# Optimization experiments

Hardware: AMD Instinct MI355X
Metric: run time of the kernel (lower is better)

The kernel has to match this reference:

```python
import jax, jax.numpy as jnp
import numpy as np

B, D_IMG, D_TXT, E = 4096, 768, 768, 512
LAMBDA_CMP = 1.0
EPS = 1e-10


def setup_inputs() -> dict:
    key = jax.random.key(0)
    k1, k2, k3, k4, k5 = jax.random.split(key, 5)
    return {
        "images": jax.random.normal(k1, (B, D_IMG), dtype=jnp.float32),
        "texts": jax.random.normal(k2, (B, D_TXT), dtype=jnp.float32),
        "labels": jax.random.randint(k3, (B,), 0, 1000, dtype=jnp.int32),
        "W_img": jax.random.normal(k4, (D_IMG, E), dtype=jnp.float32) / np.sqrt(D_IMG),
        "W_txt": jax.random.normal(k5, (D_TXT, E), dtype=jnp.float32) / np.sqrt(D_TXT),
        "logit_scale": jnp.asarray(np.log(1.0 / 0.07), dtype=jnp.float32),
    }


def reference(images, texts, labels, W_img, W_txt, logit_scale):
    # CLIP-style encoders: linear project + L2 normalize
    img = images @ W_img
    txt = texts @ W_txt
    img = img / jnp.linalg.norm(img, axis=-1, keepdims=True)
    txt = txt / jnp.linalg.norm(txt, axis=-1, keepdims=True)
    logits = jnp.exp(logit_scale) * (img @ txt.T)  # [B, B]

    b = logits.shape[0]
    rows = jnp.arange(b)
    logp = jax.nn.log_softmax(logits, axis=-1)
    clip_loss = -jnp.mean(logp[rows, labels])

    probs = jnp.exp(logp)                # softmax probs [B, B]
    p_yi = probs[rows, labels]           # [B]
    # columns j whose label differs from sample i's label AND prob exceeds p_yi
    diff_label = labels[None, :] != labels[:, None]           # [B, B]
    mask = diff_label & (probs > p_yi[:, None])               # [B, B]
    denom = jnp.sum(jnp.where(mask, probs, 0.0), axis=1)      # [B]
    has_any = jnp.any(mask, axis=1)
    cmp_loss = jnp.sum(jnp.where(has_any, p_yi / (denom + EPS), 0.0)) / b

    return clip_loss + LAMBDA_CMP * cmp_loss
```

## Files before the change

kernel.cpp:

```cpp
#include <hip/hip_runtime.h>
#include <stdint.h>

#define BATCH 4096
#define DDIM  768
#define EDIM  512
#define NSPLIT 16
#define LOG2E 1.44269504088896340736f

using short8  = __attribute__((ext_vector_type(8))) short;
using float4v = __attribute__((ext_vector_type(4))) float;

__device__ __forceinline__ unsigned short f2bf(float x) {
    union { float f; uint32_t u; } v; v.f = x;
    uint32_t u = v.u;
    u += 0x7FFFu + ((u >> 16) & 1u);
    return (unsigned short)(u >> 16);
}
__device__ __forceinline__ float bf2f(unsigned short h) {
    union { uint32_t u; float f; } v; v.u = ((uint32_t)h) << 16;
    return v.f;
}

__device__ __forceinline__ void gl2lds16(const void* g, void* l) {
    __builtin_amdgcn_global_load_lds(
        (const __attribute__((address_space(1))) void*)g,
        (__attribute__((address_space(3))) void*)l, 16, 0, 0);
}

__global__ void cvt2(const float* __restrict__ a, const float* __restrict__ b,
                     unsigned short* __restrict__ oa, unsigned short* __restrict__ ob) {
    int i = blockIdx.x * 256 + threadIdx.x;
    const float* in = blockIdx.y ? b : a;
    unsigned short* out = blockIdx.y ? ob : oa;
    float4 v = ((const float4*)in)[i];
    ushort4 o;
    o.x = f2bf(v.x); o.y = f2bf(v.y); o.z = f2bf(v.z); o.w = f2bf(v.w);
    ((ushort4*)out)[i] = o;
}

__global__ void transpose2(const float* __restrict__ Wa, const float* __restrict__ Wb,
                           unsigned short* __restrict__ Ta, unsigned short* __restrict__ Tb) {
    const float* W = blockIdx.z ? Wb : Wa;
    unsigned short* Wt = blockIdx.z ? Tb : Ta;
    __shared__ float tile[32][33];
    int n0 = blockIdx.x * 32, k0 = blockIdx.y * 32;
    int tid = threadIdx.x;
    for (int p = 0; p < 4; ++p) {
        int e = tid + p * 256; int lr = e >> 5, lc = e & 31;
        tile[lc][lr] = W[(size_t)(k0 + lr) * EDIM + n0 + lc];
    }
    __syncthreads();
    for (int p = 0; p < 4; ++p) {
        int e = tid + p * 256; int lr = e >> 5, lc = e & 31;
        Wt[(size_t)(n0 + lr) * DDIM + k0 + lc] = f2bf(tile[lr][lc]);
    }
}

__global__ __launch_bounds__(256) void gemm_nt(const unsigned short* __restrict__ Aimg,
                                               const unsigned short* __restrict__ Atxt,
                                               const unsigned short* __restrict__ Bimg,
                                               const unsigned short* __restrict__ Btxt,
                                               unsigned short* __restrict__ Cimg,
                                               unsigned short* __restrict__ Ctxt) {
    const unsigned short* A  = blockIdx.z ? Atxt : Aimg;
    const unsigned short* Bm = blockIdx.z ? Btxt : Bimg;
    unsigned short* C        = blockIdx.z ? Ctxt : Cimg;
    __shared__ __align__(16) unsigned short As[2 * 128 * 32];
    __shared__ __align__(16) unsigned short Bs[2 * 64 * 32];
    int tid = threadIdx.x;
    int wave = tid >> 6, lane = tid & 63;
    int q = lane >> 4, r = lane & 15;
    int m0 = blockIdx.x * 128, n0 = blockIdx.y * 64;
    int sw = (r >> 1) & 3;

    const unsigned short* gsA[4];
    unsigned short* lsA[4];
    for (int i = 0; i < 4; ++i) {
        int u = i * 256 + tid;
        int kc2 = u >> 9, row = (u >> 2) & 127, kq = u & 3;
        int kq2 = kq ^ ((row >> 1) & 3);
        gsA[i] = &A[(size_t)(m0 + row) * DDIM + kc2 * 32 + kq2 * 8];
        lsA[i] = &As[u * 8];
    }
    const unsigned short* gsB[2];
    unsigned short* lsB[2];
    for (int i = 0; i < 2; ++i) {
        int u = i * 256 + tid;
        int kc2 = u >> 8, row = (u >> 2) & 63, kq = u & 3;
        int kq2 = kq ^ ((row >> 1) & 3);
        gsB[i] = &Bm[(size_t)(n0 + row) * DDIM + kc2 * 32 + kq2 * 8];
        lsB[i] = &Bs[u * 8];
    }

    float4v acc[2][4];
    for (int a = 0; a < 2; ++a)
        for (int t = 0; t < 4; ++t) acc[a][t] = (float4v){0.f, 0.f, 0.f, 0.f};

    for (int it = 0; it < DDIM / 64; ++it) {
        int k0 = it * 64;
        __syncthreads();
        for (int i = 0; i < 4; ++i) gl2lds16(gsA[i] + k0, lsA[i]);
        for (int i = 0; i < 2; ++i) gl2lds16(gsB[i] + k0, lsB[i]);
        __syncthreads();
        for (int kc2 = 0; kc2 < 2; ++kc2) {
            short8 a0 = *(const short8*)&As[kc2 * 4096 + (wave * 32 + r) * 32 + (q ^ sw) * 8];
            short8 a1 = *(const short8*)&As[kc2 * 4096 + (wave * 32 + 16 + r) * 32 + (q ^ sw) * 8];
            for (int t = 0; t < 4; ++t) {
                short8 b = *(const short8*)&Bs[kc2 * 2048 + (t * 16 + r) * 32 + (q ^ sw) * 8];
                acc[0][t] = __builtin_amdgcn_mfma_f32_16x16x32_bf16(a0, b, acc[0][t], 0, 0, 0);
                acc[1][t] = __builtin_amdgcn_mfma_f32_16x16x32_bf16(a1, b, acc[1][t], 0, 0, 0);
            }
        }
    }
    for (int rg = 0; rg < 2; ++rg)
        for (int t = 0; t < 4; ++t)
            for (int g = 0; g < 4; ++g)
                C[(size_t)(m0 + wave * 32 + rg * 16 + q * 4 + g) * EDIM + n0 + t * 16 + r] =
                    f2bf(acc[rg][t][g]);
}

__global__ void norm_rows(unsigned short* __restrict__ Pa, unsigned short* __restrict__ Pb) {
    unsigned short* P = blockIdx.y ? Pb : Pa;
    int wave = threadIdx.x >> 6, lane = threadIdx.x & 63;
    int row = blockIdx.x * 4 + wave;
    unsigned short* p = &P[(size_t)row * 512 + lane * 8];
    union { unsigned short us[8]; uint4 u4; } v;
    v.u4 = *(const uint4*)p;
    float f[8], s = 0.f;
    for (int j = 0; j < 8; ++j) { f[j] = bf2f(v.us[j]); s += f[j] * f[j]; }
    for (int off = 1; off < 64; off <<= 1) s += __shfl_xor(s, off);
    float rn = rsqrtf(s);
    for (int j = 0; j < 8; ++j) v.us[j] = f2bf(f[j] * rn);
    *(uint4*)p = v.u4;
}

__global__ void tdot(const unsigned short* __restrict__ img, const unsigned short* __restrict__ txt,
                     const int* __restrict__ labels, float* __restrict__ tout) {
    int wave = threadIdx.x >> 6, lane = threadIdx.x & 63;
    int row = blockIdx.x * 4 + wave;
    int lab = labels[row];
    union { unsigned short us[8]; uint4 u4; } a, b;
    a.u4 = *(const uint4*)&img[(size_t)row * 512 + lane * 8];
    b.u4 = *(const uint4*)&txt[(size_t)lab * 512 + lane * 8];
    float s = 0.f;
    for (int j = 0; j < 8; ++j) s += bf2f(a.us[j]) * bf2f(b.us[j]);
    for (int off = 1; off < 64; off <<= 1) s += __shfl_xor(s, off);
    if (lane == 0) tout[row] = s;
}

__global__ __launch_bounds__(256) void flash_pass(
    const unsigned short* __restrict__ img, const unsigned short* __restrict__ txt,
    const int* __restrict__ labels, const float* __restrict__ tvals,
    const float* __restrict__ ls,
    float* __restrict__ lP, float* __restrict__ dP) {
    __shared__ __align__(16) unsigned short Bs[8 * 64 * 32];
    int tid = threadIdx.x;
    int wave = tid >> 6, lane = tid & 63;
    int q = lane >> 4, r = lane & 15;
    int row0 = blockIdx.x * 128 + wave * 32;
    int split = blockIdx.y;
    float alpha = expf(ls[0]);
    float c1 = alpha * LOG2E;

    int srow = tid >> 2, skp = tid & 3;
    int skp2 = skp ^ ((srow >> 1) & 3);
    int sw = (r >> 1) & 3;

    short8 af[2][16];
    for (int rg = 0; rg < 2; ++rg)
        for (int kc = 0; kc < 16; ++kc)
            af[rg][kc] = *(const short8*)&img[(size_t)(row0 + rg * 16 + r) * 512 + kc * 32 + q * 8];

    int labr[8]; float tr[8];
    for (int rg = 0; rg < 2; ++rg)
        for (int g = 0; g < 4; ++g) {
            int rw = row0 + rg * 16 + q * 4 + g;
            labr[rg * 4 + g] = labels[rw];
            tr[rg * 4 + g] = tvals[rw];
        }
    float l[8] = {0.f}, d[8] = {0.f};

    for (int ct = 0; ct < 4; ++ct) {
        int colbase = split * 256 + ct * 64;
        const unsigned short* gB = &txt[(size_t)(colbase + srow) * 512 + skp2 * 8];
        float4v acc[2][4];
        for (int rg = 0; rg < 2; ++rg)
            for (int t = 0; t < 4; ++t) acc[rg][t] = (float4v){0.f, 0.f, 0.f, 0.f};
        for (int h = 0; h < 2; ++h) {
            __syncthreads();
            for (int i = 0; i < 8; ++i)
                gl2lds16(gB + h * 256 + i * 32, &Bs[i * 2048 + tid * 8]);
            __syncthreads();
            for (int kc = 0; kc < 8; ++kc) {
                short8 a0 = af[0][h * 8 + kc];
                short8 a1 = af[1][h * 8 + kc];
                for (int t = 0; t < 4; ++t) {
                    short8 bf = *(const short8*)&Bs[(kc * 64 + t * 16 + r) * 32 + (q ^ sw) * 8];
                    acc[0][t] = __builtin_amdgcn_mfma_f32_16x16x32_bf16(a0, bf, acc[0][t], 0, 0, 0);
                    acc[1][t] = __builtin_amdgcn_mfma_f32_16x16x32_bf16(a1, bf, acc[1][t], 0, 0, 0);
                }
            }
        }
        for (int t = 0; t < 4; ++t) {
            int lc = labels[colbase + t * 16 + r];
            for (int rg = 0; rg < 2; ++rg)
                for (int g = 0; g < 4; ++g) {
                    float a = acc[rg][t][g];
                    float p = exp2f(fmaf(a, c1, -c1));
                    int ix = rg * 4 + g;
                    l[ix] += p;
                    d[ix] += ((a > tr[ix]) && (lc != labr[ix])) ? p : 0.f;
                }
        }
    }
    for (int ix = 0; ix < 8; ++ix) {
        float lv = l[ix], dv = d[ix];
        for (int off = 1; off < 16; off <<= 1) {
            lv += __shfl_xor(lv, off);
            dv += __shfl_xor(dv, off);
        }
        if (r == 0) {
            int rw = row0 + (ix >> 2) * 16 + q * 4 + (ix & 3);
            lP[(size_t)rw * NSPLIT + split] = lv;
            dP[(size_t)rw * NSPLIT + split] = dv;
        }
    }
}

__global__ void combine(const float* __restrict__ lP, const float* __restrict__ dP,
                        const float* __restrict__ tvals, const float* __restrict__ ls,
                        float* __restrict__ out) {
    int row = blockIdx.x * 256 + threadIdx.x;
    float alpha = expf(ls[0]);
    float L = 0.f, D = 0.f;
    for (int s = 0; s < NSPLIT; ++s) {
        L += lP[(size_t)row * NSPLIT + s];
        D += dP[(size_t)row * NSPLIT + s];
    }
    float tm = alpha * (tvals[row] - 1.0f);
    float clip = logf(L) - tm;
    float py = expf(tm) / L;
    float cmp = (D > 0.f) ? py / (D / L + 1e-10f) : 0.f;
    float v = clip + cmp;
    for (int off = 1; off < 64; off <<= 1) v += __shfl_xor(v, off);
    __shared__ float w4[4];
    int wave = threadIdx.x >> 6, lane = threadIdx.x & 63;
    if (lane == 0) w4[wave] = v;
    __syncthreads();
    if (threadIdx.x == 0)
        atomicAdd(out, (w4[0] + w4[1] + w4[2] + w4[3]) * (1.0f / BATCH));
}

extern "C" void kernel_launch(void* const* d_in, const int* in_sizes, int n_in,
                              void* d_out, int out_size, void* d_ws, size_t ws_size,
                              hipStream_t stream) {
    const float* images = (const float*)d_in[0];
    const float* texts  = (const float*)d_in[1];
    const int*   labels = (const int*)d_in[2];
    const float* W_img  = (const float*)d_in[3];
    const float* W_txt  = (const float*)d_in[4];
    const float* lscale = (const float*)d_in[5];
    float* out = (float*)d_out;

    char* ws = (char*)d_ws;
    unsigned short* img_bf = (unsigned short*)(ws + 0);
    unsigned short* txt_bf = (unsigned short*)(ws + 6291456);
    unsigned short* wt_img = (unsigned short*)(ws + 12582912);
    unsigned short* wt_txt = (unsigned short*)(ws + 13369344);
    unsigned short* proj_i = (unsigned short*)(ws + 14155776);
    unsigned short* proj_t = (unsigned short*)(ws + 18350080);
    float*          lP     = (float*)(ws + 0);
    float*          dP     = (float*)(ws + 262144);
    float*          tvals  = (float*)(ws + 524288);

    hipMemsetAsync(out, 0, sizeof(float), stream);
    cvt2<<<dim3(3072, 2), 256, 0, stream>>>(images, texts, img_bf, txt_bf);
    transpose2<<<dim3(EDIM / 32, DDIM / 32, 2), 256, 0, stream>>>(W_img, W_txt, wt_img, wt_txt);
    gemm_nt<<<dim3(BATCH / 128, EDIM / 64, 2), 256, 0, stream>>>(img_bf, txt_bf, wt_img, wt_txt,
                                                                 proj_i, proj_t);
    norm_rows<<<dim3(BATCH / 4, 2), 256, 0, stream>>>(proj_i, proj_t);
    tdot<<<BATCH / 4, 256, 0, stream>>>(proj_i, proj_t, labels, tvals);
    flash_pass<<<dim3(BATCH / 128, NSPLIT), 256, 0, stream>>>(proj_i, proj_t, labels, tvals, lscale,
                                                              lP, dP);
    combine<<<16, 256, 0, stream>>>(lP, dP, tvals, lscale, out);
}
```

Before: 143.6 us.

## Merge prep kernels, double flash splits, and store partials split-major

Fuses the bf16 conversion and the weight transpose into one prep kernel to save a launch. It doubles the column splits in the flash pass (32 splits of 128 columns each), which doubles the grid to 1024 blocks to improve occupancy and latency hiding. The partial sums are now stored split-major so the combine kernel reads them coalesced. In exchange, each block reloads the A fragments for half as much work, and the combine step reads twice as many partials.

Measured after the change: 170.0 us. 1.18x slower.

```diff
diff --git a/kernel.cpp b/kernel.cpp
--- a/kernel.cpp
+++ b/kernel.cpp
@@ -4,7 +4,7 @@
 #define BATCH 4096
 #define DDIM  768
 #define EDIM  512
-#define NSPLIT 16
+#define NSPLIT 32
 #define LOG2E 1.44269504088896340736f
 
 using short8  = __attribute__((ext_vector_type(8))) short;
@@ -27,32 +27,38 @@
         (__attribute__((address_space(3))) void*)l, 16, 0, 0);
 }
 
-__global__ void cvt2(const float* __restrict__ a, const float* __restrict__ b,
-                     unsigned short* __restrict__ oa, unsigned short* __restrict__ ob) {
-    int i = blockIdx.x * 256 + threadIdx.x;
-    const float* in = blockIdx.y ? b : a;
-    unsigned short* out = blockIdx.y ? ob : oa;
-    float4 v = ((const float4*)in)[i];
-    ushort4 o;
-    o.x = f2bf(v.x); o.y = f2bf(v.y); o.z = f2bf(v.z); o.w = f2bf(v.w);
-    ((ushort4*)out)[i] = o;
-}
-
-__global__ void transpose2(const float* __restrict__ Wa, const float* __restrict__ Wb,
-                           unsigned short* __restrict__ Ta, unsigned short* __restrict__ Tb) {
-    const float* W = blockIdx.z ? Wb : Wa;
-    unsigned short* Wt = blockIdx.z ? Tb : Ta;
+__global__ void prep(const float* __restrict__ images, const float* __restrict__ texts,
+                     const float* __restrict__ Wa, const float* __restrict__ Wb,
+                     unsigned short* __restrict__ img_bf, unsigned short* __restrict__ txt_bf,
+                     unsigned short* __restrict__ Ta, unsigned short* __restrict__ Tb) {
     __shared__ float tile[32][33];
-    int n0 = blockIdx.x * 32, k0 = blockIdx.y * 32;
+    int b = blockIdx.x;
     int tid = threadIdx.x;
-    for (int p = 0; p < 4; ++p) {
-        int e = tid + p * 256; int lr = e >> 5, lc = e & 31;
-        tile[lc][lr] = W[(size_t)(k0 + lr) * EDIM + n0 + lc];
-    }
-    __syncthreads();
-    for (int p = 0; p < 4; ++p) {
-        int e = tid + p * 256; int lr = e >> 5, lc = e & 31;
-        Wt[(size_t)(n0 + lr) * DDIM + k0 + lc] = f2bf(tile[lr][lc]);
+    if (b < 6144) {
+        int which = b >= 3072;
+        const float* in = which ? texts : images;
+        unsigned short* out = which ? txt_bf : img_bf;
+        int i = (which ? b - 3072 : b) * 256 + tid;
+        float4 v = ((const float4*)in)[i];
+        ushort4 o;
+        o.x = f2bf(v.x); o.y = f2bf(v.y); o.z = f2bf(v.z); o.w = f2bf(v.w);
+        ((ushort4*)out)[i] = o;
+    } else {
+        int z = b - 6144;
+        int which = z >= 384;
+        int rem = which ? z - 384 : z;
+        const float* W = which ? Wb : Wa;
+        unsigned short* Wt = which ? Tb : Ta;
+        int n0 = (rem & 15) * 32, k0 = (rem >> 4) * 32;
+        for (int p = 0; p < 4; ++p) {
+            int e = tid + p * 256; int lr = e >> 5, lc = e & 31;
+            tile[lc][lr] = W[(size_t)(k0 + lr) * EDIM + n0 + lc];
+        }
+        __syncthreads();
+        for (int p = 0; p < 4; ++p) {
+            int e = tid + p * 256; int lr = e >> 5, lc = e & 31;
+            Wt[(size_t)(n0 + lr) * DDIM + k0 + lc] = f2bf(tile[lr][lc]);
+        }
     }
 }
 
@@ -159,8 +165,7 @@
     int q = lane >> 4, r = lane & 15;
     int row0 = blockIdx.x * 128 + wave * 32;
     int split = blockIdx.y;
-    float alpha = expf(ls[0]);
-    float c1 = alpha * LOG2E;
+    float c1 = expf(ls[0]) * LOG2E;
 
     int srow = tid >> 2, skp = tid & 3;
     int skp2 = skp ^ ((srow >> 1) & 3);
@@ -180,8 +185,8 @@
         }
     float l[8] = {0.f}, d[8] = {0.f};
 
-    for (int ct = 0; ct < 4; ++ct) {
-        int colbase = split * 256 + ct * 64;
+    for (int ct = 0; ct < 2; ++ct) {
+        int colbase = split * 128 + ct * 64;
         const unsigned short* gB = &txt[(size_t)(colbase + srow) * 512 + skp2 * 8];
         float4v acc[2][4];
         for (int rg = 0; rg < 2; ++rg)
@@ -221,8 +226,8 @@
         }
         if (r == 0) {
             int rw = row0 + (ix >> 2) * 16 + q * 4 + (ix & 3);
-            lP[(size_t)rw * NSPLIT + split] = lv;
-            dP[(size_t)rw * NSPLIT + split] = dv;
+            lP[(size_t)split * BATCH + rw] = lv;
+            dP[(size_t)split * BATCH + rw] = dv;
         }
     }
 }
@@ -234,8 +239,8 @@
     float alpha = expf(ls[0]);
     float L = 0.f, D = 0.f;
     for (int s = 0; s < NSPLIT; ++s) {
-        L += lP[(size_t)row * NSPLIT + s];
-        D += dP[(size_t)row * NSPLIT + s];
+        L += lP[(size_t)s * BATCH + row];
+        D += dP[(size_t)s * BATCH + row];
     }
     float tm = alpha * (tvals[row] - 1.0f);
     float clip = logf(L) - tm;
@@ -270,12 +275,11 @@
     unsigned short* proj_i = (unsigned short*)(ws + 14155776);
     unsigned short* proj_t = (unsigned short*)(ws + 18350080);
     float*          lP     = (float*)(ws + 0);
-    float*          dP     = (float*)(ws + 262144);
-    float*          tvals  = (float*)(ws + 524288);
+    float*          dP     = (float*)(ws + 524288);
+    float*          tvals  = (float*)(ws + 1048576);
 
     hipMemsetAsync(out, 0, sizeof(float), stream);
-    cvt2<<<dim3(3072, 2), 256, 0, stream>>>(images, texts, img_bf, txt_bf);
-    transpose2<<<dim3(EDIM / 32, DDIM / 32, 2), 256, 0, stream>>>(W_img, W_txt, wt_img, wt_txt);
+    prep<<<6912, 256, 0, stream>>>(images, texts, W_img, W_txt, img_bf, txt_bf, wt_img, wt_txt);
     gemm_nt<<<dim3(BATCH / 128, EDIM / 64, 2), 256, 0, stream>>>(img_bf, txt_bf, wt_img, wt_txt,
                                                                  proj_i, proj_t);
     norm_rows<<<dim3(BATCH / 4, 2), 256, 0, stream>>>(proj_i, proj_t);
```
